# Kernel tuning notes

Hardware: AMD Instinct MI355X
Metric: run time of the kernel (lower is better)

The kernel has to match this reference:

```python
import jax, jax.numpy as jnp
import numpy as np

NF = 32      # feature channels
DG = 4       # deformable groups
K = 9        # 3x3 kernel taps


def _conv(x, w, b, stride=1):
    # x: [B,C,H,W], w: [O,I,3,3] (pad=1)
    y = jax.lax.conv_general_dilated(x, w, (stride, stride), ((1, 1), (1, 1)),
                                     dimension_numbers=('NCHW', 'OIHW', 'NCHW'))
    return y + b[None, :, None, None]


def _lrelu(x):
    return jnp.where(x >= 0, x, 0.1 * x)


def _up2(x):
    # bilinear, align_corners=False (half-pixel centers, matches torch F.interpolate)
    B, C, H, W = x.shape
    return jax.image.resize(x, (B, C, 2 * H, 2 * W), method='bilinear')


def _deform_conv(x, om, w, b):
    # Modulated deformable conv (DCNv2), stride=1, pad=1, dilation=1, 3x3.
    # x: [B,C,H,W]; om: [B,3*DG*K,H,W] = (offset_y | offset_x | mask) blocks.
    B, C, H, W = x.shape
    Cg = C // DG
    o1, o2, m = jnp.split(om, 3, axis=1)
    off_y = o1.reshape(B, DG, K, H, W)
    off_x = o2.reshape(B, DG, K, H, W)
    mask = jax.nn.sigmoid(m).reshape(B, DG, K, H, W)
    k = jnp.arange(K)
    dy = (k // 3 - 1).astype(x.dtype)            # kernel tap y displacement
    dx = (k % 3 - 1).astype(x.dtype)
    # sampling positions [B,DG,K,H,W]
    py = off_y + jnp.arange(H, dtype=x.dtype)[:, None] + dy[:, None, None]
    px = off_x + jnp.arange(W, dtype=x.dtype)[None, :] + dx[:, None, None]
    y0 = jnp.floor(py)
    x0 = jnp.floor(px)
    wy1 = py - y0
    wx1 = px - x0
    y0i = y0.astype(jnp.int32)
    x0i = x0.astype(jnp.int32)
    imgf = x.reshape(B, DG, Cg, H * W)

    def corner(yi, xi, wt):
        valid = (yi >= 0) & (yi < H) & (xi >= 0) & (xi < W)
        yc = jnp.clip(yi, 0, H - 1)
        xc = jnp.clip(xi, 0, W - 1)
        idx = (yc * W + xc).reshape(B, DG, 1, K * H * W)
        v = jnp.take_along_axis(imgf, idx, axis=3).reshape(B, DG, Cg, K, H, W)
        return v * (wt * valid)[:, :, None]

    samp = (corner(y0i, x0i, (1 - wy1) * (1 - wx1))
            + corner(y0i, x0i + 1, (1 - wy1) * wx1)
            + corner(y0i + 1, x0i, wy1 * (1 - wx1))
            + corner(y0i + 1, x0i + 1, wy1 * wx1))
    samp = samp * mask[:, :, None]                       # [B,DG,Cg,K,H,W]
    out = jnp.einsum('bgckhw,ogck->bohw', samp, w.reshape(w.shape[0], DG, Cg, K))
    return out + b[None, :, None, None]


_PARAM_SHAPES = [
    ('w1_1', (32, 64, 3, 3)), ('b1_1', (32,)),
    ('w2_1', (32, 32, 3, 3)), ('b2_1', (32,)),
    ('w3_1', (32, 32, 3, 3)), ('b3_1', (32,)),
    ('w4_1', (32, 32, 3, 3)), ('b4_1', (32,)),
    ('w6_1', (32, 32, 3, 3)), ('b6_1', (32,)),
    ('w7_1', (32, 32, 3, 3)), ('b7_1', (32,)),
    ('w1_2', (32, 64, 3, 3)), ('b1_2', (32,)),
    ('w2_2', (32, 32, 3, 3)), ('b2_2', (32,)),
    ('w3_2', (32, 64, 3, 3)), ('b3_2', (32,)),
    ('w4_2', (32, 32, 3, 3)), ('b4_2', (32,)),
    ('w_om', (108, 32, 3, 3)), ('b_om', (108,)),   # DCN_sep conv_offset_mask: 3*DG*K=108
    ('w_dcn', (32, 32, 3, 3)), ('b_dcn', (32,)),
]


def setup_inputs() -> dict:
    key = jax.random.key(0)
    ks = jax.random.split(key, len(_PARAM_SHAPES) + 2)
    B, H, W = 4, 192, 192
    d = {
        'fea1': jax.random.normal(ks[0], (B, NF, H, W), jnp.float32),
        'fea2': jax.random.normal(ks[1], (B, NF, H, W), jnp.float32),
    }
    for i, (name, shp) in enumerate(_PARAM_SHAPES):
        d[name] = jax.random.normal(ks[i + 2], shp, jnp.float32) * 0.05
    return d


def reference(fea1, fea2, w1_1, b1_1, w2_1, b2_1, w3_1, b3_1, w4_1, b4_1,
              w6_1, b6_1, w7_1, b7_1, w1_2, b1_2, w2_2, b2_2, w3_2, b3_2,
              w4_2, b4_2, w_om, b_om, w_dcn, b_dcn):
    off = _lrelu(_conv(jnp.concatenate([fea1, fea2], 1), w1_1, b1_1))
    off1 = _lrelu(_conv(off, w2_1, b2_1))
    off2 = _lrelu(_conv(off1, w3_1, b3_1, 2))   # H/2
    off2 = _lrelu(_conv(off2, w4_1, b4_1))
    off3 = _lrelu(_conv(off2, w6_1, b6_1, 2))   # H/4
    off3 = _lrelu(_conv(off3, w7_1, b7_1))
    up = _up2(off3)                              # back to H/2
    off = _lrelu(_conv(jnp.concatenate([up, off2], 1), w1_2, b1_2))
    off = _lrelu(_conv(off, w2_2, b2_2))
    up = _up2(off)                               # back to H
    off = _lrelu(_conv(jnp.concatenate([up, off1], 1), w3_2, b3_2))
    base_offset = _conv(off, w4_2, b4_2)
    om = _conv(base_offset, w_om, b_om)          # DCN_sep offset/mask head
    return _deform_conv(fea2, om, w_dcn, b_dcn)
```

## Files before the change

kernel.cpp:

```cpp
#include <hip/hip_runtime.h>
#include <math.h>


#define BDIM 256

typedef __attribute__((ext_vector_type(8))) short short8v;
typedef __attribute__((ext_vector_type(4))) float f32x4;

__device__ __forceinline__ unsigned short f2bf(float f) {
    unsigned u = __builtin_bit_cast(unsigned, f);
    u = (u + 0x7FFF + ((u >> 16) & 1)) >> 16;
    return (unsigned short)u;
}
__device__ __forceinline__ float bf2f(unsigned short h) {
    unsigned u = ((unsigned)h) << 16;
    return __builtin_bit_cast(float, u);
}

template<int NPASS, bool LRELU, int YS>
__global__ __launch_bounds__(BDIM, NPASS == 1 ? 4 : 3)
void convr_k(const short* __restrict__ in0, const short* __restrict__ in1,
             const short* __restrict__ wf,
             const float* __restrict__ bias,
             short* __restrict__ out, int H, int W)
{
    const int lane = threadIdx.x & 63;
    const int wid  = blockIdx.x * 4 + (threadIdx.x >> 6);
    const int hh   = wid & 1;
    const int sw   = wid >> 1;
    const int segs = W >> 4;
    const int strips = (H / YS) * segs;
    const int b = sw / strips;
    int r = sw - b * strips;
    const int ys = r / segs;
    const int y0 = ys * YS;
    const int x0 = (r - ys * segs) * 16;
    const int lp = lane & 15;
    const int g  = lane >> 4;

    int colOff[3]; bool colOk[3];
#pragma unroll
    for (int tx = 0; tx < 3; ++tx) {
        const int ix = x0 + lp + tx - 1;
        colOk[tx] = (unsigned)ix < (unsigned)W;
        colOff[tx] = min(max(ix, 0), W - 1) * 32 + g * 8;
    }

    const size_t inPlane = (size_t)H * W * 32;
    const short8v zero = {};
    const short* inp0 = in0 + (size_t)b * inPlane;
    const short* inp1 = (NPASS > 1) ? in1 + (size_t)b * inPlane : nullptr;

    short8v awc[9];
#pragma unroll
    for (int t = 0; t < 9; ++t)
        awc[t] = *(const short8v*)(wf + (((size_t)t * 2 + hh) * 64 + lane) * 8);

    short8v win[NPASS][3][3];

#define LOADROW(SLOT, IY) do {                                                \
        const int iy_ = (IY);                                                 \
        const bool rok_ = (unsigned)iy_ < (unsigned)H;                        \
        const int ro_ = min(max(iy_, 0), H - 1) * W;                          \
        _Pragma("unroll")                                                     \
        for (int tx = 0; tx < 3; ++tx) {                                      \
            short8v v_ = *(const short8v*)(inp0 + (size_t)ro_ * 32 + colOff[tx]); \
            win[0][SLOT][tx] = (rok_ & colOk[tx]) ? v_ : zero;                \
            if constexpr (NPASS > 1) {                                        \
                short8v w_ = *(const short8v*)(inp1 + (size_t)ro_ * 32 + colOff[tx]); \
                win[1][SLOT][tx] = (rok_ & colOk[tx]) ? w_ : zero;            \
            }                                                                 \
        }                                                                     \
    } while (0)

    LOADROW(0, y0 - 1);
    LOADROW(1, y0);

#pragma unroll
    for (int s = 0; s < YS; ++s) {
        LOADROW((s + 2) % 3, y0 + s + 1);

        f32x4 a0 = (f32x4){0.f, 0.f, 0.f, 0.f};
#pragma unroll
        for (int p = 0; p < NPASS; ++p) {
#pragma unroll
            for (int ty = 0; ty < 3; ++ty) {
#pragma unroll
                for (int tx = 0; tx < 3; ++tx) {
                    const int t = ty * 3 + tx;
                    const short8v bv = win[p][(s + ty) % 3][tx];
                    short8v av;
                    if (p == 0) {
                        av = awc[t];
                    } else {
                        av = *(const short8v*)(
                            wf + ((((size_t)9 + t) * 2 + hh) * 64 + lane) * 8);
                    }
                    a0 = __builtin_amdgcn_mfma_f32_16x16x32_bf16(av, bv, a0, 0, 0, 0);
                }
            }
        }

        short* op = out + (((size_t)b * H + (y0 + s)) * W + x0 + lp) * 32;
        ushort4 st0;
#pragma unroll
        for (int j = 0; j < 4; ++j) {
            float v0 = a0[j] + bias[hh * 16 + g * 4 + j];
            if (LRELU) v0 = (v0 >= 0.f) ? v0 : 0.1f * v0;
            ((unsigned short*)&st0)[j] = f2bf(v0);
        }
        *(ushort4*)(op + hh * 16 + g * 4) = st0;
    }
#undef LOADROW
}

template<int NPASS, int NHALF, int STRIDE, bool LRELU>
__global__ __launch_bounds__(BDIM, 4)
void convm_k(const short* __restrict__ in0, const short* __restrict__ in1,
             const short* __restrict__ wf,
             const float* __restrict__ bias,
             short* __restrict__ out,
             int Hin, int Win, int Hout, int Wout, int OCS)
{
    const int lane = threadIdx.x & 63;
    const int wid  = blockIdx.x * 4 + (threadIdx.x >> 6);
    const int segs = Wout >> 4;
    const int b  = wid / (Hout * segs);
    int r = wid - b * (Hout * segs);
    const int oy = r / segs;
    const int x0 = (r - oy * segs) * 16;
    const int lp = lane & 15;
    const int g  = lane >> 4;

    int rowOff[3]; bool rowOk[3];
#pragma unroll
    for (int ty = 0; ty < 3; ++ty) {
        const int iy = oy * STRIDE + ty - 1;
        rowOk[ty] = (unsigned)iy < (unsigned)Hin;
        rowOff[ty] = min(max(iy, 0), Hin - 1) * Win;
    }
    int colOff[3]; bool colOk[3];
#pragma unroll
    for (int tx = 0; tx < 3; ++tx) {
        const int ix = (x0 + lp) * STRIDE + tx - 1;
        colOk[tx] = (unsigned)ix < (unsigned)Win;
        colOff[tx] = min(max(ix, 0), Win - 1) * 32 + g * 8;
    }

    f32x4 acc[NHALF];
#pragma unroll
    for (int h = 0; h < NHALF; ++h) acc[h] = (f32x4){0.f, 0.f, 0.f, 0.f};

    const size_t inPlane = (size_t)Hin * Win * 32;
    const short8v zero = {};

#pragma unroll
    for (int pass = 0; pass < NPASS; ++pass) {
        const short* inp = (pass == 0 ? in0 : in1) + (size_t)b * inPlane;

        short8v bv[9];
#pragma unroll
        for (int t = 0; t < 9; ++t) {
            const int ty = t / 3, tx = t % 3;
            short8v v = *(const short8v*)(inp + (size_t)rowOff[ty] * 32 + colOff[tx]);
            bv[t] = (rowOk[ty] & colOk[tx]) ? v : zero;
        }
#pragma unroll
        for (int t = 0; t < 9; ++t) {
#pragma unroll
            for (int h = 0; h < NHALF; ++h) {
                short8v av = *(const short8v*)(
                    wf + ((((size_t)pass * 9 + t) * NHALF + h) * 64 + lane) * 8);
                acc[h] = __builtin_amdgcn_mfma_f32_16x16x32_bf16(av, bv[t], acc[h], 0, 0, 0);
            }
        }
    }

    short* op = out + (((size_t)b * Hout + oy) * Wout + x0 + lp) * OCS;
#pragma unroll
    for (int h = 0; h < NHALF; ++h) {
        const int co0 = h * 16 + g * 4;
        ushort4 st;
#pragma unroll
        for (int j = 0; j < 4; ++j) {
            float v = acc[h][j] + bias[co0 + j];
            if (LRELU) v = (v >= 0.f) ? v : 0.1f * v;
            ((unsigned short*)&st)[j] = f2bf(v);
        }
        *(ushort4*)(op + co0) = st;
    }
}

struct WPArgs {
    const float* src[11];
    int off[11];
    int npass[11], nhalf[11], O[11];
};

__global__ __launch_bounds__(BDIM)
void wprep_k(WPArgs a, short* __restrict__ wbase)
{
    const int z = blockIdx.z;
    const int n = a.npass[z] * 9 * a.nhalf[z] * 512;
    const int idx = blockIdx.x * BDIM + threadIdx.x;
    if (idx >= n) return;
    const int j = idx & 7;
    const int l = (idx >> 3) & 63;
    int r = idx >> 9;
    const int h = r % a.nhalf[z]; r /= a.nhalf[z];
    const int t = r % 9;
    const int pass = r / 9;
    const int I = a.npass[z] * 32;
    const int cout = h * 16 + (l & 15);
    const int cin  = pass * 32 + (l >> 4) * 8 + j;
    float v = (cout < a.O[z]) ? a.src[z][((size_t)cout * I + cin) * 9 + t] : 0.f;
    wbase[a.off[z] + idx] = (short)f2bf(v);
}

__global__ __launch_bounds__(BDIM)
void wdp_k(const float* __restrict__ w, short* __restrict__ dst)
{
    const int idx = blockIdx.x * BDIM + threadIdx.x;
    if (idx >= 9 * 2 * 64 * 8) return;
    const int j = idx & 7;
    const int l = (idx >> 3) & 63;
    const int h = (idx >> 9) & 1;
    const int k = idx >> 10;
    const int cout = h * 16 + (l & 15);
    const int cin  = (l >> 4) * 8 + j;
    dst[idx] = (short)f2bf(w[((size_t)cout * 32 + cin) * 9 + k]);
}

__global__ __launch_bounds__(BDIM)
void cvtnhwc_k(const float* __restrict__ s0, const float* __restrict__ s1,
               short* __restrict__ d0, short* __restrict__ d1, int H, int W)
{
    const float* s = blockIdx.z ? s1 : s0;
    short* d = blockIdx.z ? d1 : d0;
    const int idx = blockIdx.x * BDIM + threadIdx.x;
    if (idx >= 4 * 32 * H * W) return;
    const int c = idx & 31;
    int t = idx >> 5;
    const int x = t % W; t /= W;
    const int y = t % H;
    const int b = t / H;
    d[idx] = (short)f2bf(s[(((size_t)b * 32 + c) * H + y) * W + x]);
}

__global__ __launch_bounds__(BDIM)
void up2b_k(const short* __restrict__ in, short* __restrict__ out,
            int Hin, int Win)
{
    const int Hout = 2 * Hin, Wout = 2 * Win;
    const int idx = blockIdx.x * BDIM + threadIdx.x;
    if (idx >= 4 * Hout * Wout * 4) return;
    const int cg = idx & 3;
    int t = idx >> 2;
    const int x = t % Wout; t /= Wout;
    const int y = t % Hout;
    const int b = t / Hout;

    const float sy = (y + 0.5f) * 0.5f - 0.5f;
    const float sx = (x + 0.5f) * 0.5f - 0.5f;
    const float y0f = floorf(sy), x0f = floorf(sx);
    const float wy = sy - y0f, wx = sx - x0f;
    const int y0 = (int)y0f, x0 = (int)x0f;
    const int y0c = min(max(y0, 0), Hin - 1);
    const int y1c = min(max(y0 + 1, 0), Hin - 1);
    const int x0c = min(max(x0, 0), Win - 1);
    const int x1c = min(max(x0 + 1, 0), Win - 1);

    const short* base = in + (size_t)b * Hin * Win * 32 + cg * 8;
    short8v v00 = *(const short8v*)(base + ((size_t)y0c * Win + x0c) * 32);
    short8v v01 = *(const short8v*)(base + ((size_t)y0c * Win + x1c) * 32);
    short8v v10 = *(const short8v*)(base + ((size_t)y1c * Win + x0c) * 32);
    short8v v11 = *(const short8v*)(base + ((size_t)y1c * Win + x1c) * 32);

    short8v o;
#pragma unroll
    for (int j = 0; j < 8; ++j) {
        float f = (1.f - wy) * ((1.f - wx) * bf2f((unsigned short)v00[j]) +
                                wx * bf2f((unsigned short)v01[j]))
                + wy * ((1.f - wx) * bf2f((unsigned short)v10[j]) +
                        wx * bf2f((unsigned short)v11[j]));
        o[j] = (short)f2bf(f);
    }
    short* op = out + (size_t)b * Hout * Wout * 32 + ((size_t)y * Wout + x) * 32 + cg * 8;
    *(short8v*)op = o;
}

__global__ __launch_bounds__(BDIM, 4)
void dcnm_k(const short* __restrict__ xb,
            const short* __restrict__ bo,
            const short* __restrict__ wfo,
            const float* __restrict__ obias,
            const short* __restrict__ wfd,
            const float* __restrict__ bias,
            float* __restrict__ out, int H, int W)
{
    __shared__ unsigned short omld[4][16][116];

    const int lane = threadIdx.x & 63;
    const int wv   = threadIdx.x >> 6;
    const int wid  = blockIdx.x * 4 + wv;
    const int segs = W >> 4;
    const int b = wid / (H * segs);
    int r = wid - b * (H * segs);
    const int y = r / segs;
    const int x0 = (r - y * segs) * 16;
    const int lp = lane & 15;
    const int g  = lane >> 4;
    const int x  = x0 + lp;
    const size_t plane = (size_t)H * W;
    const short8v zero = {};

    {
        int rowOff[3]; bool rowOk[3];
#pragma unroll
        for (int ty = 0; ty < 3; ++ty) {
            const int iy = y + ty - 1;
            rowOk[ty] = (unsigned)iy < (unsigned)H;
            rowOff[ty] = min(max(iy, 0), H - 1) * W;
        }
        int colOff[3]; bool colOk[3];
#pragma unroll
        for (int tx = 0; tx < 3; ++tx) {
            const int ix = x + tx - 1;
            colOk[tx] = (unsigned)ix < (unsigned)W;
            colOff[tx] = min(max(ix, 0), W - 1) * 32 + g * 8;
        }
        const short* inp = bo + (size_t)b * plane * 32;
        short8v bv[9];
#pragma unroll
        for (int t = 0; t < 9; ++t) {
            const int ty = t / 3, tx = t % 3;
            short8v v = *(const short8v*)(inp + (size_t)rowOff[ty] * 32 + colOff[tx]);
            bv[t] = (rowOk[ty] & colOk[tx]) ? v : zero;
        }
        f32x4 acc[7];
#pragma unroll
        for (int h = 0; h < 7; ++h) acc[h] = (f32x4){0.f, 0.f, 0.f, 0.f};
#pragma unroll
        for (int t = 0; t < 9; ++t) {
#pragma unroll
            for (int h = 0; h < 7; ++h) {
                short8v av = *(const short8v*)(wfo + (((size_t)t * 7 + h) * 64 + lane) * 8);
                acc[h] = __builtin_amdgcn_mfma_f32_16x16x32_bf16(av, bv[t], acc[h], 0, 0, 0);
            }
        }
#pragma unroll
        for (int h = 0; h < 7; ++h) {
            const int co0 = h * 16 + g * 4;
            ushort4 st;
#pragma unroll
            for (int j = 0; j < 4; ++j)
                ((unsigned short*)&st)[j] = f2bf(acc[h][j] + obias[min(co0 + j, 107)]);
            *(ushort4*)&omld[wv][lp][co0] = st;
        }
    }

    f32x4 p0 = (f32x4){0.f, 0.f, 0.f, 0.f};
    f32x4 p1 = (f32x4){0.f, 0.f, 0.f, 0.f};
    const short* xbb = xb + (size_t)b * plane * 32 + g * 8;

#pragma unroll
    for (int k = 0; k < 9; ++k) {
        const float offy = bf2f(omld[wv][lp][g * 9 + k]);
        const float offx = bf2f(omld[wv][lp][36 + g * 9 + k]);
        const float ml   = bf2f(omld[wv][lp][72 + g * 9 + k]);
        const float m = 1.f / (1.f + __expf(-ml));

        const float py = offy + (float)y + (float)(k / 3 - 1);
        const float px = offx + (float)x + (float)(k % 3 - 1);
        const float y0f = floorf(py), x0f = floorf(px);
        const int y0 = (int)y0f, x0i = (int)x0f;
        const float wy1 = py - y0f, wx1 = px - x0f;
        const float wy0 = 1.f - wy1, wx0 = 1.f - wx1;

        const bool y0ok = (unsigned)y0 < (unsigned)H;
        const bool y1ok = (unsigned)(y0 + 1) < (unsigned)H;
        const bool x0ok = (unsigned)x0i < (unsigned)W;
        const bool x1ok = (unsigned)(x0i + 1) < (unsigned)W;
        const int y0c = min(max(y0, 0), H - 1);
        const int y1c = min(max(y0 + 1, 0), H - 1);
        const int x0c = min(max(x0i, 0), W - 1);
        const int x1c = min(max(x0i + 1, 0), W - 1);

        const float w00 = wy0 * wx0 * ((y0ok && x0ok) ? 1.f : 0.f) * m;
        const float w01 = wy0 * wx1 * ((y0ok && x1ok) ? 1.f : 0.f) * m;
        const float w10 = wy1 * wx0 * ((y1ok && x0ok) ? 1.f : 0.f) * m;
        const float w11 = wy1 * wx1 * ((y1ok && x1ok) ? 1.f : 0.f) * m;

        short8v v00 = *(const short8v*)(xbb + ((size_t)y0c * W + x0c) * 32);
        short8v v01 = *(const short8v*)(xbb + ((size_t)y0c * W + x1c) * 32);
        short8v v10 = *(const short8v*)(xbb + ((size_t)y1c * W + x0c) * 32);
        short8v v11 = *(const short8v*)(xbb + ((size_t)y1c * W + x1c) * 32);

        short8v bv;
#pragma unroll
        for (int j = 0; j < 8; ++j) {
            float s = w00 * bf2f((unsigned short)v00[j])
                    + w01 * bf2f((unsigned short)v01[j])
                    + w10 * bf2f((unsigned short)v10[j])
                    + w11 * bf2f((unsigned short)v11[j]);
            bv[j] = (short)f2bf(s);
        }

        short8v a0 = *(const short8v*)(wfd + (((size_t)k * 2 + 0) * 64 + lane) * 8);
        short8v a1 = *(const short8v*)(wfd + (((size_t)k * 2 + 1) * 64 + lane) * 8);
        p0 = __builtin_amdgcn_mfma_f32_16x16x32_bf16(a0, bv, p0, 0, 0, 0);
        p1 = __builtin_amdgcn_mfma_f32_16x16x32_bf16(a1, bv, p1, 0, 0, 0);
    }

    float* op = out + (size_t)b * 32 * plane + (size_t)y * W + x;
#pragma unroll
    for (int j = 0; j < 4; ++j) {
        const int co0 = g * 4 + j;
        const int co1 = 16 + g * 4 + j;
        op[(size_t)co0 * plane] = p0[j] + bias[co0];
        op[(size_t)co1 * plane] = p1[j] + bias[co1];
    }
}


extern "C" void kernel_launch(void* const* d_in, const int* in_sizes, int n_in,
                              void* d_out, int out_size, void* d_ws, size_t ws_size,
                              hipStream_t stream)
{
    const float* fea1  = (const float*)d_in[0];
    const float* fea2  = (const float*)d_in[1];
    const float* w1_1  = (const float*)d_in[2];  const float* b1_1 = (const float*)d_in[3];
    const float* w2_1  = (const float*)d_in[4];  const float* b2_1 = (const float*)d_in[5];
    const float* w3_1  = (const float*)d_in[6];  const float* b3_1 = (const float*)d_in[7];
    const float* w4_1  = (const float*)d_in[8];  const float* b4_1 = (const float*)d_in[9];
    const float* w6_1  = (const float*)d_in[10]; const float* b6_1 = (const float*)d_in[11];
    const float* w7_1  = (const float*)d_in[12]; const float* b7_1 = (const float*)d_in[13];
    const float* w1_2  = (const float*)d_in[14]; const float* b1_2 = (const float*)d_in[15];
    const float* w2_2  = (const float*)d_in[16]; const float* b2_2 = (const float*)d_in[17];
    const float* w3_2  = (const float*)d_in[18]; const float* b3_2 = (const float*)d_in[19];
    const float* w4_2  = (const float*)d_in[20]; const float* b4_2 = (const float*)d_in[21];
    const float* w_om  = (const float*)d_in[22]; const float* b_om = (const float*)d_in[23];
    const float* w_dcn = (const float*)d_in[24]; const float* b_dcn= (const float*)d_in[25];

    const int H = 192, W = 192;
    char* ws = (char*)d_ws;

    short* fea1b = (short*)(ws + 0);
    short* fea2b = (short*)(ws + 9437184);
    short* bufA  = (short*)(ws + 18874368);
    short* bufB  = (short*)(ws + 28311552);
    short* bufC  = (short*)(ws + 0);
    short* bufD  = (short*)(ws + 2359296);
    short* bufE  = (short*)(ws + 4718592);
    short* bufF  = (short*)(ws + 5308416);
    short* bufG  = (short*)(ws + 5898240);
    short* bufH  = (short*)(ws + 0);
    short* bufI  = (short*)(ws + 4718592);
    short* bufJ  = (short*)(ws + 37748736);
    short* bufK  = (short*)(ws + 18874368);
    short* bufL  = (short*)(ws + 0);
    short* wfrag = (short*)(ws + 70778880);
    short* wfdcn = (short*)(ws + 71083008);

    const int WOFF[11] = {0, 18432, 27648, 36864, 46080, 55296,
                          64512, 82944, 92160, 110592, 119808};

    dim3 blk(BDIM, 1, 1);

    {
        WPArgs a;
        const float* srcs[11] = {w1_1, w2_1, w3_1, w4_1, w6_1, w7_1,
                                 w1_2, w2_2, w3_2, w4_2, w_om};
        const int NP[11] = {2,1,1,1,1,1,2,1,2,1,1};
        const int NH[11] = {2,2,2,2,2,2,2,2,2,2,7};
        const int Os[11] = {32,32,32,32,32,32,32,32,32,32,108};
        for (int i = 0; i < 11; ++i) {
            a.src[i] = srcs[i]; a.off[i] = WOFF[i];
            a.npass[i] = NP[i]; a.nhalf[i] = NH[i]; a.O[i] = Os[i];
        }
        wprep_k<<<dim3(126, 1, 11), blk, 0, stream>>>(a, wfrag);
        cvtnhwc_k<<<dim3(18432, 1, 2), blk, 0, stream>>>(fea1, fea2, fea1b, fea2b, H, W);
        wdp_k<<<dim3(36), blk, 0, stream>>>(w_dcn, wfdcn);
    }

    convr_k<2,true,2><<<dim3(2304), blk, 0, stream>>>(
        fea1b, fea2b, wfrag + WOFF[0], b1_1, bufA, 192, 192);
    convr_k<1,true,2><<<dim3(2304), blk, 0, stream>>>(
        bufA, nullptr, wfrag + WOFF[1], b2_1, bufB, 192, 192);
    convm_k<1,2,2,true><<<dim3(576), blk, 0, stream>>>(
        bufB, nullptr, wfrag + WOFF[2], b3_1, bufC, 192,192,96,96, 32);
    convm_k<1,2,1,true><<<dim3(576), blk, 0, stream>>>(
        bufC, nullptr, wfrag + WOFF[3], b4_1, bufD, 96,96,96,96, 32);
    convm_k<1,2,2,true><<<dim3(144), blk, 0, stream>>>(
        bufD, nullptr, wfrag + WOFF[4], b6_1, bufE, 96,96,48,48, 32);
    convm_k<1,2,1,true><<<dim3(144), blk, 0, stream>>>(
        bufE, nullptr, wfrag + WOFF[5], b7_1, bufF, 48,48,48,48, 32);
    up2b_k<<<dim3(576), blk, 0, stream>>>(bufF, bufG, 48, 48);
    convm_k<2,2,1,true><<<dim3(576), blk, 0, stream>>>(
        bufG, bufD, wfrag + WOFF[6], b1_2, bufH, 96,96,96,96, 32);
    convm_k<1,2,1,true><<<dim3(576), blk, 0, stream>>>(
        bufH, nullptr, wfrag + WOFF[7], b2_2, bufI, 96,96,96,96, 32);
    up2b_k<<<dim3(2304), blk, 0, stream>>>(bufI, bufJ, 96, 96);
    convr_k<2,true,2><<<dim3(2304), blk, 0, stream>>>(
        bufJ, bufB, wfrag + WOFF[8], b3_2, bufK, 192, 192);
    convr_k<1,false,2><<<dim3(2304), blk, 0, stream>>>(
        bufK, nullptr, wfrag + WOFF[9], b4_2, bufL, 192, 192);
    dcnm_k<<<dim3(2304), blk, 0, stream>>>(
        fea2b, bufL, wfrag + WOFF[10], b_om, wfdcn, b_dcn, (float*)d_out, H, W);
}
```

Baseline: 316.5 us.

## Restructure full-res conv to per-pass loop with taller strips and packed bf16 stores

After: 299.9 us. 5.3% less time.

```diff
diff --git a/kernel.cpp b/kernel.cpp
--- a/kernel.cpp
+++ b/kernel.cpp
@@ -16,9 +16,14 @@
     unsigned u = ((unsigned)h) << 16;
     return __builtin_bit_cast(float, u);
 }
+__device__ __forceinline__ unsigned cvtpk(float a, float b) {
+    unsigned r;
+    asm("v_cvt_pk_bf16_f32 %0, %1, %2" : "=v"(r) : "v"(a), "v"(b));
+    return r;
+}
 
 template<int NPASS, bool LRELU, int YS>
-__global__ __launch_bounds__(BDIM, NPASS == 1 ? 4 : 3)
+__global__ __launch_bounds__(BDIM, 3)
 void convr_k(const short* __restrict__ in0, const short* __restrict__ in1,
              const short* __restrict__ wf,
              const float* __restrict__ bias,
@@ -48,70 +53,69 @@
 
     const size_t inPlane = (size_t)H * W * 32;
     const short8v zero = {};
-    const short* inp0 = in0 + (size_t)b * inPlane;
-    const short* inp1 = (NPASS > 1) ? in1 + (size_t)b * inPlane : nullptr;
-
-    short8v awc[9];
-#pragma unroll
-    for (int t = 0; t < 9; ++t)
-        awc[t] = *(const short8v*)(wf + (((size_t)t * 2 + hh) * 64 + lane) * 8);
-
-    short8v win[NPASS][3][3];
-
-#define LOADROW(SLOT, IY) do {                                                \
+
+    f32x4 acc[YS];
+#pragma unroll
+    for (int s = 0; s < YS; ++s) acc[s] = (f32x4){0.f, 0.f, 0.f, 0.f};
+
+#pragma unroll
+    for (int pass = 0; pass < NPASS; ++pass) {
+        const short* inp = (pass == 0 ? in0 : in1) + (size_t)b * inPlane;
+
+        short8v awc[9];
+#pragma unroll
+        for (int t = 0; t < 9; ++t)
+            awc[t] = *(const short8v*)(
+                wf + ((((size_t)pass * 9 + t) * 2 + hh) * 64 + lane) * 8);
+
+        short8v win[4][3];
+
+#define LDR(SLOT, IY) do {                                                    \
         const int iy_ = (IY);                                                 \
         const bool rok_ = (unsigned)iy_ < (unsigned)H;                        \
         const int ro_ = min(max(iy_, 0), H - 1) * W;                          \
         _Pragma("unroll")                                                     \
         for (int tx = 0; tx < 3; ++tx) {                                      \
-            short8v v_ = *(const short8v*)(inp0 + (size_t)ro_ * 32 + colOff[tx]); \
-            win[0][SLOT][tx] = (rok_ & colOk[tx]) ? v_ : zero;                \
-            if constexpr (NPASS > 1) {                                        \
-                short8v w_ = *(const short8v*)(inp1 + (size_t)ro_ * 32 + colOff[tx]); \
-                win[1][SLOT][tx] = (rok_ & colOk[tx]) ? w_ : zero;            \
-            }                                                                 \
+            short8v v_ = *(const short8v*)(inp + (size_t)ro_ * 32 + colOff[tx]); \
+            win[SLOT][tx] = (rok_ & colOk[tx]) ? v_ : zero;                   \
         }                                                                     \
     } while (0)
 
-    LOADROW(0, y0 - 1);
-    LOADROW(1, y0);
-
-#pragma unroll
-    for (int s = 0; s < YS; ++s) {
-        LOADROW((s + 2) % 3, y0 + s + 1);
-
-        f32x4 a0 = (f32x4){0.f, 0.f, 0.f, 0.f};
-#pragma unroll
-        for (int p = 0; p < NPASS; ++p) {
+        LDR(0, y0 - 1);
+        LDR(1, y0);
+        LDR(2, y0 + 1);
+
+#pragma unroll
+        for (int s = 0; s < YS; ++s) {
+            if (s <= YS - 2)
+                LDR((s + 3) & 3, y0 + s + 2);
 #pragma unroll
             for (int ty = 0; ty < 3; ++ty) {
 #pragma unroll
                 for (int tx = 0; tx < 3; ++tx) {
-                    const int t = ty * 3 + tx;
-                    const short8v bv = win[p][(s + ty) % 3][tx];
-                    short8v av;
-                    if (p == 0) {
-                        av = awc[t];
-                    } else {
-                        av = *(const short8v*)(
-                            wf + ((((size_t)9 + t) * 2 + hh) * 64 + lane) * 8);
-                    }
-                    a0 = __builtin_amdgcn_mfma_f32_16x16x32_bf16(av, bv, a0, 0, 0, 0);
+                    acc[s] = __builtin_amdgcn_mfma_f32_16x16x32_bf16(
+                        awc[ty * 3 + tx], win[(s + ty) & 3][tx], acc[s], 0, 0, 0);
                 }
             }
         }
-
+#undef LDR
+    }
+
+#pragma unroll
+    for (int s = 0; s < YS; ++s) {
         short* op = out + (((size_t)b * H + (y0 + s)) * W + x0 + lp) * 32;
-        ushort4 st0;
+        float v[4];
 #pragma unroll
         for (int j = 0; j < 4; ++j) {
-            float v0 = a0[j] + bias[hh * 16 + g * 4 + j];
-            if (LRELU) v0 = (v0 >= 0.f) ? v0 : 0.1f * v0;
-            ((unsigned short*)&st0)[j] = f2bf(v0);
-        }
-        *(ushort4*)(op + hh * 16 + g * 4) = st0;
-    }
-#undef LOADROW
+            float t = acc[s][j] + bias[hh * 16 + g * 4 + j];
+            if (LRELU) t = (t >= 0.f) ? t : 0.1f * t;
+            v[j] = t;
+        }
+        uint2 st;
+        st.x = cvtpk(v[0], v[1]);
+        st.y = cvtpk(v[2], v[3]);
+        *(uint2*)(op + hh * 16 + g * 4) = st;
+    }
 }
 
 template<int NPASS, int NHALF, int STRIDE, bool LRELU>
@@ -351,11 +355,14 @@
 #pragma unroll
         for (int h = 0; h < 7; ++h) {
             const int co0 = h * 16 + g * 4;
-            ushort4 st;
-#pragma unroll
-            for (int j = 0; j < 4; ++j)
-                ((unsigned short*)&st)[j] = f2bf(acc[h][j] + obias[min(co0 + j, 107)]);
-            *(ushort4*)&omld[wv][lp][co0] = st;
+            float t0 = acc[h][0] + obias[min(co0 + 0, 107)];
+            float t1 = acc[h][1] + obias[min(co0 + 1, 107)];
+            float t2 = acc[h][2] + obias[min(co0 + 2, 107)];
+            float t3 = acc[h][3] + obias[min(co0 + 3, 107)];
+            uint2 st;
+            st.x = cvtpk(t0, t1);
+            st.y = cvtpk(t2, t3);
+            *(uint2*)&omld[wv][lp][co0] = st;
         }
     }
 
@@ -396,20 +403,25 @@
         short8v v10 = *(const short8v*)(xbb + ((size_t)y1c * W + x0c) * 32);
         short8v v11 = *(const short8v*)(xbb + ((size_t)y1c * W + x1c) * 32);
 
-        short8v bv;
+        float s[8];
 #pragma unroll
         for (int j = 0; j < 8; ++j) {
-            float s = w00 * bf2f((unsigned short)v00[j])
-                    + w01 * bf2f((unsigned short)v01[j])
-                    + w10 * bf2f((unsigned short)v10[j])
-                    + w11 * bf2f((unsigned short)v11[j]);
-            bv[j] = (short)f2bf(s);
-        }
+            s[j] = w00 * bf2f((unsigned short)v00[j])
+                 + w01 * bf2f((unsigned short)v01[j])
+                 + w10 * bf2f((unsigned short)v10[j])
+                 + w11 * bf2f((unsigned short)v11[j]);
+        }
+        short8v bvv;
+        unsigned* bp = (unsigned*)&bvv;
+        bp[0] = cvtpk(s[0], s[1]);
+        bp[1] = cvtpk(s[2], s[3]);
+        bp[2] = cvtpk(s[4], s[5]);
+        bp[3] = cvtpk(s[6], s[7]);
 
         short8v a0 = *(const short8v*)(wfd + (((size_t)k * 2 + 0) * 64 + lane) * 8);
         short8v a1 = *(const short8v*)(wfd + (((size_t)k * 2 + 1) * 64 + lane) * 8);
-        p0 = __builtin_amdgcn_mfma_f32_16x16x32_bf16(a0, bv, p0, 0, 0, 0);
-        p1 = __builtin_amdgcn_mfma_f32_16x16x32_bf16(a1, bv, p1, 0, 0, 0);
+        p0 = __builtin_amdgcn_mfma_f32_16x16x32_bf16(a0, bvv, p0, 0, 0, 0);
+        p1 = __builtin_amdgcn_mfma_f32_16x16x32_bf16(a1, bvv, p1, 0, 0, 0);
     }
 
     float* op = out + (size_t)b * 32 * plane + (size_t)y * W + x;
@@ -483,9 +495,9 @@
         wdp_k<<<dim3(36), blk, 0, stream>>>(w_dcn, wfdcn);
     }
 
-    convr_k<2,true,2><<<dim3(2304), blk, 0, stream>>>(
+    convr_k<2,true,4><<<dim3(1152), blk, 0, stream>>>(
         fea1b, fea2b, wfrag + WOFF[0], b1_1, bufA, 192, 192);
-    convr_k<1,true,2><<<dim3(2304), blk, 0, stream>>>(
+    convr_k<1,true,4><<<dim3(1152), blk, 0, stream>>>(
         bufA, nullptr, wfrag + WOFF[1], b2_1, bufB, 192, 192);
     convm_k<1,2,2,true><<<dim3(576), blk, 0, stream>>>(
         bufB, nullptr, wfrag + WOFF[2], b3_1, bufC, 192,192,96,96, 32);
@@ -501,9 +513,9 @@
     convm_k<1,2,1,true><<<dim3(576), blk, 0, stream>>>(
         bufH, nullptr, wfrag + WOFF[7], b2_2, bufI, 96,96,96,96, 32);
     up2b_k<<<dim3(2304), blk, 0, stream>>>(bufI, bufJ, 96, 96);
-    convr_k<2,true,2><<<dim3(2304), blk, 0, stream>>>(
+    convr_k<2,true,4><<<dim3(1152), blk, 0, stream>>>(
         bufJ, bufB, wfrag + WOFF[8], b3_2, bufK, 192, 192);
-    convr_k<1,false,2><<<dim3(2304), blk, 0, stream>>>(
+    convr_k<1,false,4><<<dim3(1152), blk, 0, stream>>>(
         bufK, nullptr, wfrag + WOFF[9], b4_2, bufL, 192, 192);
     dcnm_k<<<dim3(2304), blk, 0, stream>>>(
         fea2b, bufL, wfrag + WOFF[10], b_om, wfdcn, b_dcn, (float*)d_out, H, W);
```
